# Performance work log

Hardware: AMD Instinct MI355X
Metric: run time of the kernel (lower is better)

The kernel has to match this reference:

```python
import jax, jax.numpy as jnp
import numpy as np

B, N, E = 128, 196, 2048   # batch, num_features (14x14), encoder_dim
D, A = 512, 512            # decoder_dim, attention_dim


def setup_inputs() -> dict:
    key = jax.random.key(0)
    ks = jax.random.split(key, 8)
    s_e = 1.0 / np.sqrt(E)
    s_d = 1.0 / np.sqrt(D)
    s_a = 1.0 / np.sqrt(A)
    return {
        "encoder_out": jax.random.normal(ks[0], (B, N, E), dtype=jnp.float32),
        "decoder_hidden": jax.random.normal(ks[1], (B, D), dtype=jnp.float32),
        "We": jax.random.uniform(ks[2], (E, A), jnp.float32, -s_e, s_e),
        "be": jax.random.uniform(ks[3], (A,), jnp.float32, -s_e, s_e),
        "Wd": jax.random.uniform(ks[4], (D, A), jnp.float32, -s_d, s_d),
        "bd": jax.random.uniform(ks[5], (A,), jnp.float32, -s_d, s_d),
        "Wf": jax.random.uniform(ks[6], (A, 1), jnp.float32, -s_a, s_a),
        "bf": jax.random.uniform(ks[7], (1,), jnp.float32, -s_a, s_a),
    }


def reference(encoder_out, decoder_hidden, We, be, Wd, bd, Wf, bf):
    # att1: [B,N,A] projection of encoder features
    att1 = jnp.einsum('bne,ea->bna', encoder_out, We) + be
    # att2: [B,A] projection of decoder state, broadcast over N
    att2 = decoder_hidden @ Wd + bd
    att = jnp.tanh(att1 + att2[:, None, :])          # [B,N,A]
    scores = jnp.einsum('bna,ao->bno', att, Wf) + bf  # [B,N,1]
    alpha = jax.nn.softmax(scores, axis=1)            # softmax over num_features
    context = jnp.sum(encoder_out * alpha, axis=1)    # [B,E]
    return (context, alpha)
```

## Files before the change

kernel.cpp:

```cpp
#include <hip/hip_runtime.h>
#include <hip/hip_bf16.h>
#include <stdint.h>

#define B_   128
#define N_   196
#define E_   2048
#define D_   512
#define A_   512
#define MTOT (B_ * N_)

typedef short  short8  __attribute__((ext_vector_type(8)));
typedef float  floatx4 __attribute__((ext_vector_type(4)));

__device__ __forceinline__ unsigned short f2bf(float f) {
    union { float f; uint32_t u; } v; v.f = f;
    uint32_t r = v.u + 0x7FFFu + ((v.u >> 16) & 1u);
    return (unsigned short)(r >> 16);
}

__device__ __forceinline__ uint32_t pkbf(float a, float b) {
    uint32_t ua = __float_as_uint(a) + 0x8000u;
    uint32_t ub = __float_as_uint(b) + 0x8000u;
    return __builtin_amdgcn_perm(ub, ua, 0x07060302u);
}

__global__ void transcvt_k(const float* __restrict__ We, unsigned short* __restrict__ WeT) {
    __shared__ float tile[32][33];
    const int e0 = blockIdx.x * 32, a0 = blockIdx.y * 32;
    const int t = threadIdx.x, tc = t & 31, tr = t >> 5;
#pragma unroll
    for (int i = 0; i < 4; ++i) {
        int r = tr + i * 8;
        tile[r][tc] = We[(size_t)(e0 + r) * A_ + a0 + tc];
    }
    __syncthreads();
#pragma unroll
    for (int i = 0; i < 4; ++i) {
        int r = tr + i * 8;
        WeT[(size_t)(a0 + r) * E_ + e0 + tc] = f2bf(tile[tc][r]);
    }
}

__launch_bounds__(512)
__global__ void att2_k(const float* __restrict__ dh, const float* __restrict__ Wd,
                       const float* __restrict__ bd, const float* __restrict__ be,
                       float* __restrict__ att2p) {
    const int b = blockIdx.x, t = threadIdx.x;
    __shared__ float sdh[D_];
    sdh[t] = dh[b * D_ + t];
    __syncthreads();
    float acc = 0.f;
#pragma unroll 8
    for (int d = 0; d < D_; ++d) acc += sdh[d] * Wd[(size_t)d * A_ + t];
    att2p[(size_t)b * A_ + t] = acc + bd[t] + be[t];
}

__launch_bounds__(256, 4)
__global__ void score_gemm(const float* __restrict__ enc,
                           const unsigned short* __restrict__ WeT,
                           const float* __restrict__ att2p,
                           const float* __restrict__ Wf,
                           float* __restrict__ scoresP) {
    __shared__ __align__(16) char sMem[24576];
    __shared__ float sPart[2][128];

    const int t   = threadIdx.x;
    const int w   = t >> 6;
    const int l   = t & 63;
    const int l15 = l & 15;
    const int q4  = l >> 4;
    const int wr  = w >> 1, wc = w & 1;

    const int v     = (blockIdx.x & 7) * 98 + (blockIdx.x >> 3);
    const int strip = v >> 2, colb = v & 3;
    const int row0  = strip * 128;
    const int c0    = colb * 128;

    floatx4 acc[4][4] = {};

    const float* aSrc[4];
    int aDst[4];
#pragma unroll
    for (int j = 0; j < 4; ++j) {
        int s = (w * 4 + j) * 64 + l;
        int r = s >> 3, pc = s & 7;
        aSrc[j] = enc + (size_t)(row0 + r) * E_ + ((pc ^ (r & 7)) * 4);
        aDst[j] = (w * 4 + j) * 1024;
    }

    const unsigned short* bSrc[2];
    int bDst[2];
#pragma unroll
    for (int j = 0; j < 2; ++j) {
        int s = w * 2 + j;
        int n = s * 16 + (l >> 2), p = l & 3;
        int q = p ^ ((n >> 1) & 3);
        bSrc[j] = WeT + (size_t)(c0 + n) * E_ + q * 8;
        bDst[j] = 16384 + s * 1024;
    }

    const int pLo    = (2 * q4) ^ (l15 & 7);
    const int offAlo = (wr * 64 + l15) * 128 + pLo * 16;
    const int offAhi = (wr * 64 + l15) * 128 + (pLo ^ 1) * 16;
    const int chB    = q4 ^ ((l15 >> 1) & 3);
    const int offB   = 16384 + (wc * 64 + l15) * 64 + chB * 16;

#pragma unroll 2
    for (int kk = 0; kk < 64; ++kk) {
#pragma unroll
        for (int j = 0; j < 4; ++j)
            __builtin_amdgcn_global_load_lds(
                (const __attribute__((address_space(1))) uint32_t*)(aSrc[j] + kk * 32),
                (__attribute__((address_space(3))) uint32_t*)(sMem + aDst[j]), 16, 0, 0);
#pragma unroll
        for (int j = 0; j < 2; ++j)
            __builtin_amdgcn_global_load_lds(
                (const __attribute__((address_space(1))) uint32_t*)(bSrc[j] + kk * 32),
                (__attribute__((address_space(3))) uint32_t*)(sMem + bDst[j]), 16, 0, 0);
        __syncthreads();

        short8 bfr[4];
        union { uint32_t u[4]; short8 s; } af[4];
#pragma unroll
        for (int ni = 0; ni < 4; ++ni)
            bfr[ni] = *(const short8*)(sMem + offB + ni * 1024);
#pragma unroll
        for (int mi = 0; mi < 4; ++mi) {
            float4 lo = *(const float4*)(sMem + offAlo + mi * 2048);
            float4 hi = *(const float4*)(sMem + offAhi + mi * 2048);
            af[mi].u[0] = pkbf(lo.x, lo.y);
            af[mi].u[1] = pkbf(lo.z, lo.w);
            af[mi].u[2] = pkbf(hi.x, hi.y);
            af[mi].u[3] = pkbf(hi.z, hi.w);
        }
#pragma unroll
        for (int mi = 0; mi < 4; ++mi) {
            acc[mi][0] = __builtin_amdgcn_mfma_f32_16x16x32_bf16(af[mi].s, bfr[0], acc[mi][0], 0, 0, 0);
            acc[mi][1] = __builtin_amdgcn_mfma_f32_16x16x32_bf16(af[mi].s, bfr[1], acc[mi][1], 0, 0, 0);
            acc[mi][2] = __builtin_amdgcn_mfma_f32_16x16x32_bf16(af[mi].s, bfr[2], acc[mi][2], 0, 0, 0);
            acc[mi][3] = __builtin_amdgcn_mfma_f32_16x16x32_bf16(af[mi].s, bfr[3], acc[mi][3], 0, 0, 0);
        }
        __syncthreads();
    }

    const int cbase = c0 + wc * 64;
    float wfv[4];
#pragma unroll
    for (int ni = 0; ni < 4; ++ni) wfv[ni] = Wf[cbase + ni * 16 + l15];

#pragma unroll
    for (int mi = 0; mi < 4; ++mi) {
#pragma unroll
        for (int r = 0; r < 4; ++r) {
            const int m    = wr * 64 + mi * 16 + q4 * 4 + r;
            const int grow = row0 + m;
            const int bb   = grow / N_;
            const float* a2p = att2p + (size_t)bb * A_ + cbase;
            float s = 0.f;
#pragma unroll
            for (int ni = 0; ni < 4; ++ni) {
                float vv = acc[mi][ni][r] + a2p[ni * 16 + l15];
                float e  = __expf(2.f * vv);
                float th = 1.f - 2.f / (e + 1.f);
                s += th * wfv[ni];
            }
            s += __shfl_xor(s, 1);
            s += __shfl_xor(s, 2);
            s += __shfl_xor(s, 4);
            s += __shfl_xor(s, 8);
            if (l15 == 0) sPart[wc][m] = s;
        }
    }
    __syncthreads();
    if (t < 128) {
        scoresP[(size_t)colb * MTOT + row0 + t] = sPart[0][t] + sPart[1][t];
    }
}

__launch_bounds__(256)
__global__ void ctx_sm_k(const float* __restrict__ enc, const float* __restrict__ sp,
                         float* __restrict__ alpha, float* __restrict__ ctx) {
    const int chunk = blockIdx.x, b = blockIdx.y;
    const int t = threadIdx.x, w = t >> 6, l = t & 63;
    const int tn = t >> 6, tc = t & 63;
    __shared__ float  sAl[N_];
    __shared__ float  red[8];
    __shared__ float4 sRed[256];

    float v = -3.0e38f;
    if (t < N_) {
        const int i = b * N_ + t;
        v = sp[i] + sp[MTOT + i] + sp[2 * MTOT + i] + sp[3 * MTOT + i];
    }
    float m = v;
#pragma unroll
    for (int off = 32; off >= 1; off >>= 1) m = fmaxf(m, __shfl_xor(m, off));
    if (l == 0) red[w] = m;
    __syncthreads();
    m = fmaxf(fmaxf(red[0], red[1]), fmaxf(red[2], red[3]));
    float e = 0.f;
    if (t < N_) e = __expf(v - m);
    float s = e;
#pragma unroll
    for (int off = 32; off >= 1; off >>= 1) s += __shfl_xor(s, off);
    if (l == 0) red[4 + w] = s;
    __syncthreads();
    s = red[4] + red[5] + red[6] + red[7];
    if (t < N_) {
        float al = e / s;
        sAl[t] = al;
        if (chunk == 0) alpha[b * N_ + t] = al;
    }
    __syncthreads();

    const float* base = enc + (size_t)b * N_ * E_ + chunk * 256 + tc * 4;
    float4 a = make_float4(0.f, 0.f, 0.f, 0.f);
#pragma unroll 7
    for (int n = tn; n < N_; n += 4) {
        float  al = sAl[n];
        float4 vv = *(const float4*)(base + (size_t)n * E_);
        a.x += al * vv.x; a.y += al * vv.y; a.z += al * vv.z; a.w += al * vv.w;
    }
    sRed[t] = a;
    __syncthreads();
    if (t < 64) {
        float4 r0 = sRed[t], r1 = sRed[t + 64], r2 = sRed[t + 128], r3 = sRed[t + 192];
        float4 o = make_float4(r0.x + r1.x + r2.x + r3.x, r0.y + r1.y + r2.y + r3.y,
                               r0.z + r1.z + r2.z + r3.z, r0.w + r1.w + r2.w + r3.w);
        *(float4*)(ctx + (size_t)b * E_ + chunk * 256 + t * 4) = o;
    }
}

extern "C" void kernel_launch(void* const* d_in, const int* in_sizes, int n_in,
                              void* d_out, int out_size, void* d_ws, size_t ws_size,
                              hipStream_t stream) {
    const float* enc = (const float*)d_in[0];
    const float* dh  = (const float*)d_in[1];
    const float* We  = (const float*)d_in[2];
    const float* be  = (const float*)d_in[3];
    const float* Wd  = (const float*)d_in[4];
    const float* bd  = (const float*)d_in[5];
    const float* Wf  = (const float*)d_in[6];

    float* out   = (float*)d_out;
    float* ctx   = out;
    float* alpha = out + B_ * E_;

    char* ws = (char*)d_ws;
    unsigned short* WeT  = (unsigned short*)ws;
    float* att2p         = (float*)(ws + (2u << 20));
    float* scoresP       = (float*)(ws + (2u << 20) + (256u << 10));

    transcvt_k <<<dim3(E_ / 32, A_ / 32), 256, 0, stream>>>(We, WeT);
    att2_k     <<<dim3(B_),              512, 0, stream>>>(dh, Wd, bd, be, att2p);
    score_gemm <<<dim3(4 * MTOT / 128),  256, 0, stream>>>(enc, WeT, att2p, Wf, scoresP);
    ctx_sm_k   <<<dim3(E_ / 256, B_),    256, 0, stream>>>(enc, scoresP, alpha, ctx);
}
```

Baseline: 430.3 us.

## Pre-convert encoder to bf16 and double-buffer LDS in score GEMM

Adds a streaming kernel that converts the fp32 encoder tensor to bf16 once into workspace, so the score GEMM loads half the bytes per tile and skips the per-tile fp32-to-bf16 packing. The GEMM now double-buffers its LDS tiles, issuing the next k-tile's global-to-LDS loads before the current tile's MFMAs, with one barrier per iteration. The cost is an extra full read of the 205 MB encoder plus a 103 MB bf16 write, and the path runs only when the workspace is large enough. Otherwise the old fp32 GEMM is kept as a fallback.

New measurement: 460.5 us. 7.0% more time.

```diff
diff --git a/kernel.cpp b/kernel.cpp
--- a/kernel.cpp
+++ b/kernel.cpp
@@ -22,6 +22,20 @@
     uint32_t ua = __float_as_uint(a) + 0x8000u;
     uint32_t ub = __float_as_uint(b) + 0x8000u;
     return __builtin_amdgcn_perm(ub, ua, 0x07060302u);
+}
+
+__launch_bounds__(256)
+__global__ void cvt_enc_k(const float* __restrict__ enc, unsigned short* __restrict__ encB) {
+    const size_t total = (size_t)MTOT * E_ / 8;
+    for (size_t i = (size_t)blockIdx.x * 256 + threadIdx.x; i < total;
+         i += (size_t)gridDim.x * 256) {
+        const float4 a = ((const float4*)enc)[2 * i];
+        const float4 b = ((const float4*)enc)[2 * i + 1];
+        uint4 o;
+        o.x = pkbf(a.x, a.y); o.y = pkbf(a.z, a.w);
+        o.z = pkbf(b.x, b.y); o.w = pkbf(b.z, b.w);
+        ((uint4*)encB)[i] = o;
+    }
 }
 
 __global__ void transcvt_k(const float* __restrict__ We, unsigned short* __restrict__ WeT) {
@@ -56,12 +70,12 @@
 }
 
 __launch_bounds__(256, 4)
-__global__ void score_gemm(const float* __restrict__ enc,
-                           const unsigned short* __restrict__ WeT,
-                           const float* __restrict__ att2p,
-                           const float* __restrict__ Wf,
-                           float* __restrict__ scoresP) {
-    __shared__ __align__(16) char sMem[24576];
+__global__ void score_gemm_bf(const unsigned short* __restrict__ encB,
+                              const unsigned short* __restrict__ WeT,
+                              const float* __restrict__ att2p,
+                              const float* __restrict__ Wf,
+                              float* __restrict__ scoresP) {
+    __shared__ __align__(16) char sMem[2 * 16384];
     __shared__ float sPart[2][128];
 
     const int t   = threadIdx.x;
@@ -78,69 +92,68 @@
 
     floatx4 acc[4][4] = {};
 
-    const float* aSrc[4];
-    int aDst[4];
-#pragma unroll
-    for (int j = 0; j < 4; ++j) {
-        int s = (w * 4 + j) * 64 + l;
-        int r = s >> 3, pc = s & 7;
-        aSrc[j] = enc + (size_t)(row0 + r) * E_ + ((pc ^ (r & 7)) * 4);
-        aDst[j] = (w * 4 + j) * 1024;
-    }
-
+    const unsigned short* aSrc[2];
     const unsigned short* bSrc[2];
-    int bDst[2];
+    int aDst[2], bDst[2];
 #pragma unroll
     for (int j = 0; j < 2; ++j) {
-        int s = w * 2 + j;
-        int n = s * 16 + (l >> 2), p = l & 3;
+        int s = (w * 2 + j) * 64 + l;
+        int n = s >> 2, p = s & 3;
         int q = p ^ ((n >> 1) & 3);
-        bSrc[j] = WeT + (size_t)(c0 + n) * E_ + q * 8;
-        bDst[j] = 16384 + s * 1024;
-    }
-
-    const int pLo    = (2 * q4) ^ (l15 & 7);
-    const int offAlo = (wr * 64 + l15) * 128 + pLo * 16;
-    const int offAhi = (wr * 64 + l15) * 128 + (pLo ^ 1) * 16;
-    const int chB    = q4 ^ ((l15 >> 1) & 3);
-    const int offB   = 16384 + (wc * 64 + l15) * 64 + chB * 16;
-
+        aSrc[j] = encB + (size_t)(row0 + n) * E_ + q * 8;
+        bSrc[j] = WeT  + (size_t)(c0   + n) * E_ + q * 8;
+        aDst[j] = (w * 2 + j) * 1024;
+        bDst[j] = 8192 + (w * 2 + j) * 1024;
+    }
+
+    const int chR  = q4 ^ ((l15 >> 1) & 3);
+    const int offA = (wr * 64 + l15) * 64 + chR * 16;
+    const int offB = 8192 + (wc * 64 + l15) * 64 + chR * 16;
+
+#pragma unroll
+    for (int j = 0; j < 2; ++j) {
+        __builtin_amdgcn_global_load_lds(
+            (const __attribute__((address_space(1))) uint32_t*)(aSrc[j]),
+            (__attribute__((address_space(3))) uint32_t*)(sMem + aDst[j]), 16, 0, 0);
+        __builtin_amdgcn_global_load_lds(
+            (const __attribute__((address_space(1))) uint32_t*)(bSrc[j]),
+            (__attribute__((address_space(3))) uint32_t*)(sMem + bDst[j]), 16, 0, 0);
+    }
+    __syncthreads();
+
+    int cur = 0;
 #pragma unroll 2
     for (int kk = 0; kk < 64; ++kk) {
-#pragma unroll
-        for (int j = 0; j < 4; ++j)
+        const int nxt = cur ^ 16384;
+        const int kn  = (kk + 1) & 63;
+
+#pragma unroll
+        for (int j = 0; j < 2; ++j) {
             __builtin_amdgcn_global_load_lds(
-                (const __attribute__((address_space(1))) uint32_t*)(aSrc[j] + kk * 32),
-                (__attribute__((address_space(3))) uint32_t*)(sMem + aDst[j]), 16, 0, 0);
-#pragma unroll
-        for (int j = 0; j < 2; ++j)
+                (const __attribute__((address_space(1))) uint32_t*)(aSrc[j] + kn * 32),
+                (__attribute__((address_space(3))) uint32_t*)(sMem + nxt + aDst[j]), 16, 0, 0);
             __builtin_amdgcn_global_load_lds(
-                (const __attribute__((address_space(1))) uint32_t*)(bSrc[j] + kk * 32),
-                (__attribute__((address_space(3))) uint32_t*)(sMem + bDst[j]), 16, 0, 0);
+                (const __attribute__((address_space(1))) uint32_t*)(bSrc[j] + kn * 32),
+                (__attribute__((address_space(3))) uint32_t*)(sMem + nxt + bDst[j]), 16, 0, 0);
+        }
+
+        short8 bfr[4], afr[4];
+#pragma unroll
+        for (int ni = 0; ni < 4; ++ni)
+            bfr[ni] = *(const short8*)(sMem + cur + offB + ni * 1024);
+#pragma unroll
+        for (int mi = 0; mi < 4; ++mi)
+            afr[mi] = *(const short8*)(sMem + cur + offA + mi * 1024);
+#pragma unroll
+        for (int mi = 0; mi < 4; ++mi) {
+            acc[mi][0] = __builtin_amdgcn_mfma_f32_16x16x32_bf16(afr[mi], bfr[0], acc[mi][0], 0, 0, 0);
+            acc[mi][1] = __builtin_amdgcn_mfma_f32_16x16x32_bf16(afr[mi], bfr[1], acc[mi][1], 0, 0, 0);
+            acc[mi][2] = __builtin_amdgcn_mfma_f32_16x16x32_bf16(afr[mi], bfr[2], acc[mi][2], 0, 0, 0);
+            acc[mi][3] = __builtin_amdgcn_mfma_f32_16x16x32_bf16(afr[mi], bfr[3], acc[mi][3], 0, 0, 0);
+        }
+
         __syncthreads();
-
-        short8 bfr[4];
-        union { uint32_t u[4]; short8 s; } af[4];
-#pragma unroll
-        for (int ni = 0; ni < 4; ++ni)
-            bfr[ni] = *(const short8*)(sMem + offB + ni * 1024);
-#pragma unroll
-        for (int mi = 0; mi < 4; ++mi) {
-            float4 lo = *(const float4*)(sMem + offAlo + mi * 2048);
-            float4 hi = *(const float4*)(sMem + offAhi + mi * 2048);
-            af[mi].u[0] = pkbf(lo.x, lo.y);
-            af[mi].u[1] = pkbf(lo.z, lo.w);
-            af[mi].u[2] = pkbf(hi.x, hi.y);
-            af[mi].u[3] = pkbf(hi.z, hi.w);
-        }
-#pragma unroll
-        for (int mi = 0; mi < 4; ++mi) {
-            acc[mi][0] = __builtin_amdgcn_mfma_f32_16x16x32_bf16(af[mi].s, bfr[0], acc[mi][0], 0, 0, 0);
-            acc[mi][1] = __builtin_amdgcn_mfma_f32_16x16x32_bf16(af[mi].s, bfr[1], acc[mi][1], 0, 0, 0);
-            acc[mi][2] = __builtin_amdgcn_mfma_f32_16x16x32_bf16(af[mi].s, bfr[2], acc[mi][2], 0, 0, 0);
-            acc[mi][3] = __builtin_amdgcn_mfma_f32_16x16x32_bf16(af[mi].s, bfr[3], acc[mi][3], 0, 0, 0);
-        }
-        __syncthreads();
+        cur = nxt;
     }
 
     const int cbase = c0 + wc * 64;
@@ -177,6 +190,125 @@
     }
 }
 
+__launch_bounds__(256, 4)
+__global__ void score_gemm_f32(const float* __restrict__ enc,
+                               const unsigned short* __restrict__ WeT,
+                               const float* __restrict__ att2p,
+                               const float* __restrict__ Wf,
+                               float* __restrict__ scoresP) {
+    __shared__ __align__(16) char sMem[24576];
+    __shared__ float sPart[2][128];
+
+    const int t   = threadIdx.x;
+    const int w   = t >> 6;
+    const int l   = t & 63;
+    const int l15 = l & 15;
+    const int q4  = l >> 4;
+    const int wr  = w >> 1, wc = w & 1;
+
+    const int v     = (blockIdx.x & 7) * 98 + (blockIdx.x >> 3);
+    const int strip = v >> 2, colb = v & 3;
+    const int row0  = strip * 128;
+    const int c0    = colb * 128;
+
+    floatx4 acc[4][4] = {};
+
+    const float* aSrc[4];
+    int aDst[4];
+#pragma unroll
+    for (int j = 0; j < 4; ++j) {
+        int s = (w * 4 + j) * 64 + l;
+        int r = s >> 3, pc = s & 7;
+        aSrc[j] = enc + (size_t)(row0 + r) * E_ + ((pc ^ (r & 7)) * 4);
+        aDst[j] = (w * 4 + j) * 1024;
+    }
+    const unsigned short* bSrc[2];
+    int bDst[2];
+#pragma unroll
+    for (int j = 0; j < 2; ++j) {
+        int s = w * 2 + j;
+        int n = s * 16 + (l >> 2), p = l & 3;
+        int q = p ^ ((n >> 1) & 3);
+        bSrc[j] = WeT + (size_t)(c0 + n) * E_ + q * 8;
+        bDst[j] = 16384 + s * 1024;
+    }
+    const int pLo    = (2 * q4) ^ (l15 & 7);
+    const int offAlo = (wr * 64 + l15) * 128 + pLo * 16;
+    const int offAhi = (wr * 64 + l15) * 128 + (pLo ^ 1) * 16;
+    const int chB    = q4 ^ ((l15 >> 1) & 3);
+    const int offB   = 16384 + (wc * 64 + l15) * 64 + chB * 16;
+
+#pragma unroll 2
+    for (int kk = 0; kk < 64; ++kk) {
+#pragma unroll
+        for (int j = 0; j < 4; ++j)
+            __builtin_amdgcn_global_load_lds(
+                (const __attribute__((address_space(1))) uint32_t*)(aSrc[j] + kk * 32),
+                (__attribute__((address_space(3))) uint32_t*)(sMem + aDst[j]), 16, 0, 0);
+#pragma unroll
+        for (int j = 0; j < 2; ++j)
+            __builtin_amdgcn_global_load_lds(
+                (const __attribute__((address_space(1))) uint32_t*)(bSrc[j] + kk * 32),
+                (__attribute__((address_space(3))) uint32_t*)(sMem + bDst[j]), 16, 0, 0);
+        __syncthreads();
+
+        short8 bfr[4];
+        union { uint32_t u[4]; short8 s; } af[4];
+#pragma unroll
+        for (int ni = 0; ni < 4; ++ni)
+            bfr[ni] = *(const short8*)(sMem + offB + ni * 1024);
+#pragma unroll
+        for (int mi = 0; mi < 4; ++mi) {
+            float4 lo = *(const float4*)(sMem + offAlo + mi * 2048);
+            float4 hi = *(const float4*)(sMem + offAhi + mi * 2048);
+            af[mi].u[0] = pkbf(lo.x, lo.y);
+            af[mi].u[1] = pkbf(lo.z, lo.w);
+            af[mi].u[2] = pkbf(hi.x, hi.y);
+            af[mi].u[3] = pkbf(hi.z, hi.w);
+        }
+#pragma unroll
+        for (int mi = 0; mi < 4; ++mi) {
+            acc[mi][0] = __builtin_amdgcn_mfma_f32_16x16x32_bf16(af[mi].s, bfr[0], acc[mi][0], 0, 0, 0);
+            acc[mi][1] = __builtin_amdgcn_mfma_f32_16x16x32_bf16(af[mi].s, bfr[1], acc[mi][1], 0, 0, 0);
+            acc[mi][2] = __builtin_amdgcn_mfma_f32_16x16x32_bf16(af[mi].s, bfr[2], acc[mi][2], 0, 0, 0);
+            acc[mi][3] = __builtin_amdgcn_mfma_f32_16x16x32_bf16(af[mi].s, bfr[3], acc[mi][3], 0, 0, 0);
+        }
+        __syncthreads();
+    }
+
+    const int cbase = c0 + wc * 64;
+    float wfv[4];
+#pragma unroll
+    for (int ni = 0; ni < 4; ++ni) wfv[ni] = Wf[cbase + ni * 16 + l15];
+#pragma unroll
+    for (int mi = 0; mi < 4; ++mi) {
+#pragma unroll
+        for (int r = 0; r < 4; ++r) {
+            const int m    = wr * 64 + mi * 16 + q4 * 4 + r;
+            const int grow = row0 + m;
+            const int bb   = grow / N_;
+            const float* a2p = att2p + (size_t)bb * A_ + cbase;
+            float s = 0.f;
+#pragma unroll
+            for (int ni = 0; ni < 4; ++ni) {
+                float vv = acc[mi][ni][r] + a2p[ni * 16 + l15];
+                float e  = __expf(2.f * vv);
+                float th = 1.f - 2.f / (e + 1.f);
+                s += th * wfv[ni];
+            }
+            s += __shfl_xor(s, 1);
+            s += __shfl_xor(s, 2);
+            s += __shfl_xor(s, 4);
+            s += __shfl_xor(s, 8);
+            if (l15 == 0) sPart[wc][m] = s;
+        }
+    }
+    __syncthreads();
+    if (t < 128) {
+        scoresP[(size_t)colb * MTOT + row0 + t] = sPart[0][t] + sPart[1][t];
+    }
+}
+
 __launch_bounds__(256)
 __global__ void ctx_sm_k(const float* __restrict__ enc, const float* __restrict__ sp,
                          float* __restrict__ alpha, float* __restrict__ ctx) {
@@ -250,9 +382,17 @@
     unsigned short* WeT  = (unsigned short*)ws;
     float* att2p         = (float*)(ws + (2u << 20));
     float* scoresP       = (float*)(ws + (2u << 20) + (256u << 10));
+    unsigned short* encB = (unsigned short*)(ws + (4u << 20));
+
+    const size_t need = (4u << 20) + (size_t)MTOT * E_ * 2;
 
     transcvt_k <<<dim3(E_ / 32, A_ / 32), 256, 0, stream>>>(We, WeT);
     att2_k     <<<dim3(B_),              512, 0, stream>>>(dh, Wd, bd, be, att2p);
-    score_gemm <<<dim3(4 * MTOT / 128),  256, 0, stream>>>(enc, WeT, att2p, Wf, scoresP);
+    if (ws_size >= need) {
+        cvt_enc_k    <<<dim3(2048),          256, 0, stream>>>(enc, encB);
+        score_gemm_bf<<<dim3(4 * MTOT / 128), 256, 0, stream>>>(encB, WeT, att2p, Wf, scoresP);
+    } else {
+        score_gemm_f32<<<dim3(4 * MTOT / 128), 256, 0, stream>>>(enc, WeT, att2p, Wf, scoresP);
+    }
     ctx_sm_k   <<<dim3(E_ / 256, B_),    256, 0, stream>>>(enc, scoresP, alpha, ctx);
 }
```
